# Kernel optimization log

Measured on AMD Instinct MI355X. Metric: run time of the kernel, lower is better.

Reference implementation:

```python
import jax, jax.numpy as jnp
import numpy as np

N = 100000      # nodes
E = 1600000     # edges
D_IN, D_H, D_OUT = 256, 64, 47


def setup_inputs() -> dict:
    key = jax.random.key(0)
    k0, k1, k2, k3 = jax.random.split(key, 4)
    x = jax.random.normal(k0, (N, D_IN), dtype=jnp.float32)
    edge_index = jax.random.randint(k1, (2, E), 0, N, dtype=jnp.int64)
    W1 = jax.random.normal(k2, (D_IN, D_H), dtype=jnp.float32) / np.sqrt(D_IN)
    b1 = jnp.zeros((D_H,), dtype=jnp.float32)
    W2 = jax.random.normal(k3, (D_H, D_OUT), dtype=jnp.float32) / np.sqrt(D_H)
    b2 = jnp.zeros((D_OUT,), dtype=jnp.float32)
    return {"x": x, "edge_index": edge_index, "W1": W1, "b1": b1, "W2": W2, "b2": b2}


def _gcn_conv(x, W, b, src, dst, norm):
    # PyG GCNConv: h = x @ W, then scatter_add(norm * h[src] -> dst), + bias
    h = x @ W                                     # [N, out]
    msg = norm[:, None] * h[src]                  # [E+N, out] gather
    out = jax.ops.segment_sum(msg, dst, num_segments=N)  # scatter-add
    return out + b


def reference(x, edge_index, W1, b1, W2, b2):
    # add self-loops with weight 1 (PyG default, edge_weight=None -> ones)
    loop = jnp.arange(N, dtype=edge_index.dtype)
    src = jnp.concatenate([edge_index[0], loop])
    dst = jnp.concatenate([edge_index[1], loop])
    w = jnp.ones((E + N,), dtype=x.dtype)
    # symmetric normalization: deg^-1/2[src] * w * deg^-1/2[dst]
    deg = jax.ops.segment_sum(w, dst, num_segments=N)
    dinv = jnp.where(deg > 0, jax.lax.rsqrt(deg), 0.0)
    norm = dinv[src] * w * dinv[dst]              # [E+N]

    h = _gcn_conv(x, W1, b1, src, dst, norm)
    h = jax.nn.relu(h)
    # F.dropout(training=self.training): eval mode -> identity
    xo = _gcn_conv(h, W2, b2, src, dst, norm)     # [N, D_OUT]
    logits = jax.nn.softmax(xo, axis=1)           # nn.Softmax() -> dim=1 for 2D
    preds = jnp.argmax(logits, axis=1)
    return (logits, preds, xo)
```

## Files before the change

kernel.cpp:

```cpp
#include <hip/hip_runtime.h>
#include <math.h>

#define NN 100000
#define NE 1600000
#define DI 256
#define DH 64
#define DO 47
#define DH3 48
#define PAD 48
#define RSZ8 ((NN + 7) / 8)
#define EPB 2048
#define CPB ((NE + EPB - 1) / EPB)

__global__ __launch_bounds__(256) void k_fill1(const int* __restrict__ src,
                                               const int* __restrict__ dst,
                                               int* __restrict__ deg,
                                               int* __restrict__ csr_pad) {
    int r = blockIdx.x & 7;
    int chunk = blockIdx.x >> 3;
    int lo = r * RSZ8, hi = min(lo + RSZ8, NN);
    int base = chunk * EPB + threadIdx.x;
    #pragma unroll
    for (int i = 0; i < EPB / 256; ++i) {
        int e = base + i * 256;
        if (e < NE) {
            int d = dst[e];
            if (d >= lo && d < hi) {
                int p = atomicAdd(&deg[d], 1);
                if (p < PAD) csr_pad[d * PAD + p] = src[e];
            }
        }
    }
}

__global__ __launch_bounds__(512) void k_gemm1(const float* __restrict__ x,
                                               const float* __restrict__ W1,
                                               const int* __restrict__ deg,
                                               float* __restrict__ h1s) {
    __shared__ float xs[2][128 * 33];
    __shared__ float wl[2][32 * 64];
    const int t = threadIdx.x;
    const int lane = t & 63;
    const int wvu = __builtin_amdgcn_readfirstlane(t >> 6);
    const int r0 = blockIdx.x * 128;
    const int sr = t >> 2;
    const int sk = (t & 3) * 8;
    const int wk = t >> 4;
    const int wc = (t & 15) * 4;
    const long xrow = (long)min(r0 + sr, NN - 1) * DI;
    const int rowA = r0 + lane;
    const int rowB = r0 + 64 + lane;

    float accA[8] = {0.f, 0.f, 0.f, 0.f, 0.f, 0.f, 0.f, 0.f};
    float accB[8] = {0.f, 0.f, 0.f, 0.f, 0.f, 0.f, 0.f, 0.f};

    {
        float4 v0 = *(const float4*)(x + xrow + sk);
        float4 v1 = *(const float4*)(x + xrow + sk + 4);
        float* p = &xs[0][sr * 33 + sk];
        p[0] = v0.x; p[1] = v0.y; p[2] = v0.z; p[3] = v0.w;
        p[4] = v1.x; p[5] = v1.y; p[6] = v1.z; p[7] = v1.w;
        float4 w = *(const float4*)(W1 + (size_t)wk * DH + wc);
        float* q = &wl[0][wk * 64 + wc];
        q[0] = w.x; q[1] = w.y; q[2] = w.z; q[3] = w.w;
    }
    __syncthreads();
    for (int c = 0; c < 8; ++c) {
        const int buf = c & 1;
        if (c + 1 < 8) {
            float4 v0 = *(const float4*)(x + xrow + (c + 1) * 32 + sk);
            float4 v1 = *(const float4*)(x + xrow + (c + 1) * 32 + sk + 4);
            float* p = &xs[buf ^ 1][sr * 33 + sk];
            p[0] = v0.x; p[1] = v0.y; p[2] = v0.z; p[3] = v0.w;
            p[4] = v1.x; p[5] = v1.y; p[6] = v1.z; p[7] = v1.w;
            float4 w = *(const float4*)(W1 + (size_t)((c + 1) * 32 + wk) * DH + wc);
            float* q = &wl[buf ^ 1][wk * 64 + wc];
            q[0] = w.x; q[1] = w.y; q[2] = w.z; q[3] = w.w;
        }
        #pragma unroll 4
        for (int kk = 0; kk < 32; ++kk) {
            float xa = xs[buf][lane * 33 + kk];
            float xb = xs[buf][(lane + 64) * 33 + kk];
            const float4* wp = (const float4*)&wl[buf][kk * 64 + wvu * 8];
            float4 wa = wp[0], wb = wp[1];
            accA[0] += wa.x * xa; accA[1] += wa.y * xa;
            accA[2] += wa.z * xa; accA[3] += wa.w * xa;
            accA[4] += wb.x * xa; accA[5] += wb.y * xa;
            accA[6] += wb.z * xa; accA[7] += wb.w * xa;
            accB[0] += wa.x * xb; accB[1] += wa.y * xb;
            accB[2] += wa.z * xb; accB[3] += wa.w * xb;
            accB[4] += wb.x * xb; accB[5] += wb.y * xb;
            accB[6] += wb.z * xb; accB[7] += wb.w * xb;
        }
        __syncthreads();
    }
    if (rowA < NN) {
        float di = rsqrtf((float)(deg[rowA] + 1));
        float4 o0 = {di * accA[0], di * accA[1], di * accA[2], di * accA[3]};
        float4 o1 = {di * accA[4], di * accA[5], di * accA[6], di * accA[7]};
        float4* hp = (float4*)(h1s + (long)rowA * DH + wvu * 8);
        hp[0] = o0;
        hp[1] = o1;
    }
    if (rowB < NN) {
        float di = rsqrtf((float)(deg[rowB] + 1));
        float4 o0 = {di * accB[0], di * accB[1], di * accB[2], di * accB[3]};
        float4 o1 = {di * accB[4], di * accB[5], di * accB[6], di * accB[7]};
        float4* hp = (float4*)(h1s + (long)rowB * DH + wvu * 8);
        hp[0] = o0;
        hp[1] = o1;
    }
}

__global__ __launch_bounds__(256) void k_agg1(const int* __restrict__ deg,
                                              const int* __restrict__ csr_pad,
                                              const float* __restrict__ h1s,
                                              const float* __restrict__ b1,
                                              const float* __restrict__ W2,
                                              float* __restrict__ h3s) {
    __shared__ float w2[DH * DO];
    __shared__ float sh[8][DH];
    for (int i = threadIdx.x; i < DH * DO; i += 256) w2[i] = W2[i];
    __syncthreads();
    const int wv = threadIdx.x >> 6, lane = threadIdx.x & 63;
    const int c = lane & 15, e = lane >> 4;
    const unsigned c4 = (unsigned)(c * 4);
    const int rA = blockIdx.x * 8 + wv * 2, rB = rA + 1;
    const int degA = deg[rA], degB = deg[rB];
    const int cntA = min(degA, PAD), cntB = min(degB, PAD);
    const unsigned baseA = (unsigned)rA * PAD, baseB = (unsigned)rB * PAD;
    float aAx = 0.f, aAy = 0.f, aAz = 0.f, aAw = 0.f;
    float aBx = 0.f, aBy = 0.f, aBz = 0.f, aBw = 0.f;
    const int cmin = min(cntA, cntB), tmax = max(cntA, cntB);
    int j = 0;
    for (; j + 7 < cmin; j += 8) {
        unsigned sa0 = (unsigned)csr_pad[baseA + j + e];
        unsigned sb0 = (unsigned)csr_pad[baseB + j + e];
        unsigned sa1 = (unsigned)csr_pad[baseA + j + 4 + e];
        unsigned sb1 = (unsigned)csr_pad[baseB + j + 4 + e];
        float4 va0 = *(const float4*)(h1s + sa0 * 64u + c4);
        float4 vb0 = *(const float4*)(h1s + sb0 * 64u + c4);
        float4 va1 = *(const float4*)(h1s + sa1 * 64u + c4);
        float4 vb1 = *(const float4*)(h1s + sb1 * 64u + c4);
        aAx += va0.x + va1.x; aAy += va0.y + va1.y;
        aAz += va0.z + va1.z; aAw += va0.w + va1.w;
        aBx += vb0.x + vb1.x; aBy += vb0.y + vb1.y;
        aBz += vb0.z + vb1.z; aBw += vb0.w + vb1.w;
    }
    for (; j < tmax; j += 4) {
        int slot = min(j + e, PAD - 1);
        unsigned sa = min((unsigned)csr_pad[baseA + slot], (unsigned)(NN - 1));
        unsigned sb = min((unsigned)csr_pad[baseB + slot], (unsigned)(NN - 1));
        float4 va = *(const float4*)(h1s + sa * 64u + c4);
        float4 vb = *(const float4*)(h1s + sb * 64u + c4);
        float mA = (j + e < cntA) ? 1.f : 0.f;
        float mB = (j + e < cntB) ? 1.f : 0.f;
        aAx = fmaf(mA, va.x, aAx); aAy = fmaf(mA, va.y, aAy);
        aAz = fmaf(mA, va.z, aAz); aAw = fmaf(mA, va.w, aAw);
        aBx = fmaf(mB, vb.x, aBx); aBy = fmaf(mB, vb.y, aBy);
        aBz = fmaf(mB, vb.z, aBz); aBw = fmaf(mB, vb.w, aBw);
    }
    aAx += __shfl_xor(aAx, 16); aAx += __shfl_xor(aAx, 32);
    aAy += __shfl_xor(aAy, 16); aAy += __shfl_xor(aAy, 32);
    aAz += __shfl_xor(aAz, 16); aAz += __shfl_xor(aAz, 32);
    aAw += __shfl_xor(aAw, 16); aAw += __shfl_xor(aAw, 32);
    aBx += __shfl_xor(aBx, 16); aBx += __shfl_xor(aBx, 32);
    aBy += __shfl_xor(aBy, 16); aBy += __shfl_xor(aBy, 32);
    aBz += __shfl_xor(aBz, 16); aBz += __shfl_xor(aBz, 32);
    aBw += __shfl_xor(aBw, 16); aBw += __shfl_xor(aBw, 32);
    const float diA = rsqrtf((float)(degA + 1));
    const float diB = rsqrtf((float)(degB + 1));
    if (lane < 16) {
        float4 sA = *(const float4*)(h1s + (unsigned)rA * 64u + c4);
        float4 sB = *(const float4*)(h1s + (unsigned)rB * 64u + c4);
        float4 bb = *(const float4*)(b1 + c4);
        float4 oA, oB;
        oA.x = fmaxf(diA * (aAx + sA.x) + bb.x, 0.f);
        oA.y = fmaxf(diA * (aAy + sA.y) + bb.y, 0.f);
        oA.z = fmaxf(diA * (aAz + sA.z) + bb.z, 0.f);
        oA.w = fmaxf(diA * (aAw + sA.w) + bb.w, 0.f);
        oB.x = fmaxf(diB * (aBx + sB.x) + bb.x, 0.f);
        oB.y = fmaxf(diB * (aBy + sB.y) + bb.y, 0.f);
        oB.z = fmaxf(diB * (aBz + sB.z) + bb.z, 0.f);
        oB.w = fmaxf(diB * (aBw + sB.w) + bb.w, 0.f);
        *(float4*)&sh[wv * 2 + 0][c4] = oA;
        *(float4*)&sh[wv * 2 + 1][c4] = oB;
    }
    __syncthreads();
    if (lane < DO) {
        float oA = 0.f, oB = 0.f;
        #pragma unroll 8
        for (int k = 0; k < DH; ++k) {
            float w = w2[k * DO + lane];
            oA += sh[wv * 2 + 0][k] * w;
            oB += sh[wv * 2 + 1][k] * w;
        }
        h3s[(unsigned)rA * DH3 + lane] = diA * oA;
        h3s[(unsigned)rB * DH3 + lane] = diB * oB;
    }
}

__global__ __launch_bounds__(256) void k_agg2(const int* __restrict__ deg,
                                              const int* __restrict__ csr_pad,
                                              const float* __restrict__ h3s,
                                              const float* __restrict__ b2,
                                              float* __restrict__ logits,
                                              float* __restrict__ preds,
                                              float* __restrict__ xo) {
    const int wv = threadIdx.x >> 6, lane = threadIdx.x & 63;
    const int c = lane & 15, e = lane >> 4;
    const unsigned cc4 = (unsigned)(((c < 12) ? c : 0) * 4);
    const int rA = blockIdx.x * 8 + wv * 2, rB = rA + 1;
    const int degA = deg[rA], degB = deg[rB];
    const int cntA = min(degA, PAD), cntB = min(degB, PAD);
    const unsigned baseA = (unsigned)rA * PAD, baseB = (unsigned)rB * PAD;
    float aAx = 0.f, aAy = 0.f, aAz = 0.f, aAw = 0.f;
    float aBx = 0.f, aBy = 0.f, aBz = 0.f, aBw = 0.f;
    const int cmin = min(cntA, cntB), tmax = max(cntA, cntB);
    int j = 0;
    for (; j + 7 < cmin; j += 8) {
        unsigned sa0 = (unsigned)csr_pad[baseA + j + e];
        unsigned sb0 = (unsigned)csr_pad[baseB + j + e];
        unsigned sa1 = (unsigned)csr_pad[baseA + j + 4 + e];
        unsigned sb1 = (unsigned)csr_pad[baseB + j + 4 + e];
        float4 va0 = *(const float4*)(h3s + sa0 * 48u + cc4);
        float4 vb0 = *(const float4*)(h3s + sb0 * 48u + cc4);
        float4 va1 = *(const float4*)(h3s + sa1 * 48u + cc4);
        float4 vb1 = *(const float4*)(h3s + sb1 * 48u + cc4);
        aAx += va0.x + va1.x; aAy += va0.y + va1.y;
        aAz += va0.z + va1.z; aAw += va0.w + va1.w;
        aBx += vb0.x + vb1.x; aBy += vb0.y + vb1.y;
        aBz += vb0.z + vb1.z; aBw += vb0.w + vb1.w;
    }
    for (; j < tmax; j += 4) {
        int slot = min(j + e, PAD - 1);
        unsigned sa = min((unsigned)csr_pad[baseA + slot], (unsigned)(NN - 1));
        unsigned sb = min((unsigned)csr_pad[baseB + slot], (unsigned)(NN - 1));
        float4 va = *(const float4*)(h3s + sa * 48u + cc4);
        float4 vb = *(const float4*)(h3s + sb * 48u + cc4);
        float mA = (j + e < cntA) ? 1.f : 0.f;
        float mB = (j + e < cntB) ? 1.f : 0.f;
        aAx = fmaf(mA, va.x, aAx); aAy = fmaf(mA, va.y, aAy);
        aAz = fmaf(mA, va.z, aAz); aAw = fmaf(mA, va.w, aAw);
        aBx = fmaf(mB, vb.x, aBx); aBy = fmaf(mB, vb.y, aBy);
        aBz = fmaf(mB, vb.z, aBz); aBw = fmaf(mB, vb.w, aBw);
    }
    aAx += __shfl_xor(aAx, 16); aAx += __shfl_xor(aAx, 32);
    aAy += __shfl_xor(aAy, 16); aAy += __shfl_xor(aAy, 32);
    aAz += __shfl_xor(aAz, 16); aAz += __shfl_xor(aAz, 32);
    aAw += __shfl_xor(aAw, 16); aAw += __shfl_xor(aAw, 32);
    aBx += __shfl_xor(aBx, 16); aBx += __shfl_xor(aBx, 32);
    aBy += __shfl_xor(aBy, 16); aBy += __shfl_xor(aBy, 32);
    aBz += __shfl_xor(aBz, 16); aBz += __shfl_xor(aBz, 32);
    aBw += __shfl_xor(aBw, 16); aBw += __shfl_xor(aBw, 32);
    const float diA = rsqrtf((float)(degA + 1));
    const float diB = rsqrtf((float)(degB + 1));
    const bool lv = (lane < 16) && (c < 12);
    float b0 = 0.f, bq1 = 0.f, bq2 = 0.f, bq3 = 0.f;
    if (lv) {
        b0 = b2[c * 4 + 0]; bq1 = b2[c * 4 + 1]; bq2 = b2[c * 4 + 2];
        bq3 = (c < 11) ? b2[c * 4 + 3] : 0.f;
    }
    #pragma unroll
    for (int rr = 0; rr < 2; ++rr) {
        const int row = rr ? rB : rA;
        const float di = rr ? diB : diA;
        float ax = rr ? aBx : aAx, ay = rr ? aBy : aAy;
        float az = rr ? aBz : aAz, aw = rr ? aBw : aAw;
        float vx = -INFINITY, vy = -INFINITY, vz = -INFINITY, vw = -INFINITY;
        if (lv) {
            float4 sf = *(const float4*)(h3s + (unsigned)row * 48u + cc4);
            vx = di * (ax + sf.x) + b0;
            vy = di * (ay + sf.y) + bq1;
            vz = di * (az + sf.z) + bq2;
            vw = (c < 11) ? (di * (aw + sf.w) + bq3) : -INFINITY;
            float* xp = xo + (size_t)row * DO + c * 4;
            xp[0] = vx; xp[1] = vy; xp[2] = vz;
            if (c < 11) xp[3] = vw;
        }
        float lm = fmaxf(fmaxf(vx, vy), fmaxf(vz, vw));
        float gm = lm;
        for (int off = 32; off; off >>= 1) gm = fmaxf(gm, __shfl_xor(gm, off));
        int cand = 1 << 30;
        if (lv) {
            if (vx == gm) cand = c * 4 + 0;
            else if (vy == gm) cand = c * 4 + 1;
            else if (vz == gm) cand = c * 4 + 2;
            else if (c < 11 && vw == gm) cand = c * 4 + 3;
        }
        for (int off = 32; off; off >>= 1) cand = min(cand, __shfl_xor(cand, off));
        float e0 = 0.f, e1 = 0.f, e2 = 0.f, e3 = 0.f;
        if (lv) {
            e0 = expf(vx - gm); e1 = expf(vy - gm); e2 = expf(vz - gm);
            e3 = (c < 11) ? expf(vw - gm) : 0.f;
        }
        float gs = e0 + e1 + e2 + e3;
        for (int off = 32; off; off >>= 1) gs += __shfl_xor(gs, off);
        if (lv) {
            float* lp = logits + (size_t)row * DO + c * 4;
            lp[0] = e0 / gs; lp[1] = e1 / gs; lp[2] = e2 / gs;
            if (c < 11) lp[3] = e3 / gs;
        }
        if (lane == 0) preds[row] = (float)cand;
    }
}

extern "C" void kernel_launch(void* const* d_in, const int* in_sizes, int n_in,
                              void* d_out, int out_size, void* d_ws, size_t ws_size,
                              hipStream_t stream) {
    const float* x  = (const float*)d_in[0];
    const int*   ei = (const int*)d_in[1];
    const float* W1 = (const float*)d_in[2];
    const float* b1 = (const float*)d_in[3];
    const float* W2 = (const float*)d_in[4];
    const float* b2 = (const float*)d_in[5];
    const int* src = ei;
    const int* dst = ei + NE;

    float* out    = (float*)d_out;
    float* logits = out;
    float* preds  = out + (size_t)NN * DO;
    float* xo     = preds + NN;

    char* wsb = (char*)d_ws;
    int*   deg     = (int*)wsb;                         wsb += (size_t)NN * 4;
    int*   csr_pad = (int*)wsb;                         wsb += (size_t)NN * PAD * 4;
    float* h1s     = (float*)wsb;                       wsb += (size_t)NN * DH * 4;
    float* h3s     = (float*)wsb;                       wsb += (size_t)NN * DH3 * 4;

    hipMemsetAsync(deg, 0, NN * sizeof(int), stream);

    k_fill1<<<8 * CPB, 256, 0, stream>>>(src, dst, deg, csr_pad);
    k_gemm1<<<(NN + 127) / 128, 512, 0, stream>>>(x, W1, deg, h1s);
    k_agg1<<<NN / 8, 256, 0, stream>>>(deg, csr_pad, h1s, b1, W2, h3s);
    k_agg2<<<NN / 8, 256, 0, stream>>>(deg, csr_pad, h3s, b2, logits, preds, xo);
}
```

Before: 291.7 us.

## Sort nodes by degree and aggregate four same-degree rows per wave

Adds a degree histogram, prefix scan and counting sort that builds a node order grouped by in-degree. Both aggregation kernels now have each wave handle four rows taken from that order instead of two consecutive rows. Rows in a wave then have similar neighbour counts, which cuts the masked tail iterations and raises the number of independent gathers in flight. The cost is three extra small kernel launches and scattered, non-coalesced output writes, since rows are processed in permuted order.

Measured after the change: 577.9 us. 98.1% more time.

```diff
diff --git a/kernel.cpp b/kernel.cpp
--- a/kernel.cpp
+++ b/kernel.cpp
@@ -8,6 +8,8 @@
 #define DO 47
 #define DH3 48
 #define PAD 48
+#define BINS 64
+#define NB ((NN + 255) / 256)
 #define RSZ8 ((NN + 7) / 8)
 #define EPB 2048
 #define CPB ((NE + EPB - 1) / EPB)
@@ -30,6 +32,39 @@
                 if (p < PAD) csr_pad[d * PAD + p] = src[e];
             }
         }
+    }
+}
+
+__global__ __launch_bounds__(256) void k_hist(const int* __restrict__ deg,
+                                              int* __restrict__ bins) {
+    __shared__ int lb[BINS];
+    if (threadIdx.x < BINS) lb[threadIdx.x] = 0;
+    __syncthreads();
+    int i = blockIdx.x * 256 + threadIdx.x;
+    if (i < NN) atomicAdd(&lb[min(deg[i], BINS - 1)], 1);
+    __syncthreads();
+    if (threadIdx.x < BINS && lb[threadIdx.x])
+        atomicAdd(&bins[threadIdx.x], lb[threadIdx.x]);
+}
+
+__global__ __launch_bounds__(64) void k_prefix(int* __restrict__ bins) {
+    int t = threadIdx.x;
+    int v0 = bins[t];
+    int v = v0;
+    for (int off = 1; off < 64; off <<= 1) {
+        int u = __shfl_up(v, off);
+        if (t >= off) v += u;
+    }
+    bins[t] = v - v0;
+}
+
+__global__ __launch_bounds__(256) void k_order(const int* __restrict__ deg,
+                                               int* __restrict__ bins,
+                                               int* __restrict__ order) {
+    int i = blockIdx.x * 256 + threadIdx.x;
+    if (i < NN) {
+        int p = atomicAdd(&bins[min(deg[i], BINS - 1)], 1);
+        order[p] = i;
     }
 }
 
@@ -113,94 +148,96 @@
 }
 
 __global__ __launch_bounds__(256) void k_agg1(const int* __restrict__ deg,
+                                              const int* __restrict__ order,
                                               const int* __restrict__ csr_pad,
                                               const float* __restrict__ h1s,
                                               const float* __restrict__ b1,
                                               const float* __restrict__ W2,
                                               float* __restrict__ h3s) {
     __shared__ float w2[DH * DO];
-    __shared__ float sh[8][DH];
+    __shared__ float sh[16][DH];
     for (int i = threadIdx.x; i < DH * DO; i += 256) w2[i] = W2[i];
     __syncthreads();
     const int wv = threadIdx.x >> 6, lane = threadIdx.x & 63;
     const int c = lane & 15, e = lane >> 4;
     const unsigned c4 = (unsigned)(c * 4);
-    const int rA = blockIdx.x * 8 + wv * 2, rB = rA + 1;
-    const int degA = deg[rA], degB = deg[rB];
-    const int cntA = min(degA, PAD), cntB = min(degB, PAD);
-    const unsigned baseA = (unsigned)rA * PAD, baseB = (unsigned)rB * PAD;
-    float aAx = 0.f, aAy = 0.f, aAz = 0.f, aAw = 0.f;
-    float aBx = 0.f, aBy = 0.f, aBz = 0.f, aBw = 0.f;
-    const int cmin = min(cntA, cntB), tmax = max(cntA, cntB);
+    const int qbase = blockIdx.x * 16 + wv * 4;
+    int row[4], dg[4], cnt[4];
+    unsigned base[4];
+    #pragma unroll
+    for (int r = 0; r < 4; ++r) {
+        row[r] = order[qbase + r];
+        dg[r] = deg[row[r]];
+        cnt[r] = min(dg[r], PAD);
+        base[r] = (unsigned)row[r] * PAD;
+    }
+    float ax[4] = {0.f, 0.f, 0.f, 0.f}, ay[4] = {0.f, 0.f, 0.f, 0.f};
+    float az[4] = {0.f, 0.f, 0.f, 0.f}, aw[4] = {0.f, 0.f, 0.f, 0.f};
+    const int cmin = min(min(cnt[0], cnt[1]), min(cnt[2], cnt[3]));
+    const int tmax = max(max(cnt[0], cnt[1]), max(cnt[2], cnt[3]));
     int j = 0;
     for (; j + 7 < cmin; j += 8) {
-        unsigned sa0 = (unsigned)csr_pad[baseA + j + e];
-        unsigned sb0 = (unsigned)csr_pad[baseB + j + e];
-        unsigned sa1 = (unsigned)csr_pad[baseA + j + 4 + e];
-        unsigned sb1 = (unsigned)csr_pad[baseB + j + 4 + e];
-        float4 va0 = *(const float4*)(h1s + sa0 * 64u + c4);
-        float4 vb0 = *(const float4*)(h1s + sb0 * 64u + c4);
-        float4 va1 = *(const float4*)(h1s + sa1 * 64u + c4);
-        float4 vb1 = *(const float4*)(h1s + sb1 * 64u + c4);
-        aAx += va0.x + va1.x; aAy += va0.y + va1.y;
-        aAz += va0.z + va1.z; aAw += va0.w + va1.w;
-        aBx += vb0.x + vb1.x; aBy += vb0.y + vb1.y;
-        aBz += vb0.z + vb1.z; aBw += vb0.w + vb1.w;
+        #pragma unroll
+        for (int g = 0; g < 2; ++g) {
+            #pragma unroll
+            for (int r = 0; r < 4; ++r) {
+                unsigned s = (unsigned)csr_pad[base[r] + j + g * 4 + e];
+                float4 v = *(const float4*)(h1s + s * 64u + c4);
+                ax[r] += v.x; ay[r] += v.y; az[r] += v.z; aw[r] += v.w;
+            }
+        }
     }
     for (; j < tmax; j += 4) {
         int slot = min(j + e, PAD - 1);
-        unsigned sa = min((unsigned)csr_pad[baseA + slot], (unsigned)(NN - 1));
-        unsigned sb = min((unsigned)csr_pad[baseB + slot], (unsigned)(NN - 1));
-        float4 va = *(const float4*)(h1s + sa * 64u + c4);
-        float4 vb = *(const float4*)(h1s + sb * 64u + c4);
-        float mA = (j + e < cntA) ? 1.f : 0.f;
-        float mB = (j + e < cntB) ? 1.f : 0.f;
-        aAx = fmaf(mA, va.x, aAx); aAy = fmaf(mA, va.y, aAy);
-        aAz = fmaf(mA, va.z, aAz); aAw = fmaf(mA, va.w, aAw);
-        aBx = fmaf(mB, vb.x, aBx); aBy = fmaf(mB, vb.y, aBy);
-        aBz = fmaf(mB, vb.z, aBz); aBw = fmaf(mB, vb.w, aBw);
-    }
-    aAx += __shfl_xor(aAx, 16); aAx += __shfl_xor(aAx, 32);
-    aAy += __shfl_xor(aAy, 16); aAy += __shfl_xor(aAy, 32);
-    aAz += __shfl_xor(aAz, 16); aAz += __shfl_xor(aAz, 32);
-    aAw += __shfl_xor(aAw, 16); aAw += __shfl_xor(aAw, 32);
-    aBx += __shfl_xor(aBx, 16); aBx += __shfl_xor(aBx, 32);
-    aBy += __shfl_xor(aBy, 16); aBy += __shfl_xor(aBy, 32);
-    aBz += __shfl_xor(aBz, 16); aBz += __shfl_xor(aBz, 32);
-    aBw += __shfl_xor(aBw, 16); aBw += __shfl_xor(aBw, 32);
-    const float diA = rsqrtf((float)(degA + 1));
-    const float diB = rsqrtf((float)(degB + 1));
+        #pragma unroll
+        for (int r = 0; r < 4; ++r) {
+            unsigned s = min((unsigned)csr_pad[base[r] + slot], (unsigned)(NN - 1));
+            float4 v = *(const float4*)(h1s + s * 64u + c4);
+            float m = (j + e < cnt[r]) ? 1.f : 0.f;
+            ax[r] = fmaf(m, v.x, ax[r]); ay[r] = fmaf(m, v.y, ay[r]);
+            az[r] = fmaf(m, v.z, az[r]); aw[r] = fmaf(m, v.w, aw[r]);
+        }
+    }
+    #pragma unroll
+    for (int r = 0; r < 4; ++r) {
+        ax[r] += __shfl_xor(ax[r], 16); ax[r] += __shfl_xor(ax[r], 32);
+        ay[r] += __shfl_xor(ay[r], 16); ay[r] += __shfl_xor(ay[r], 32);
+        az[r] += __shfl_xor(az[r], 16); az[r] += __shfl_xor(az[r], 32);
+        aw[r] += __shfl_xor(aw[r], 16); aw[r] += __shfl_xor(aw[r], 32);
+    }
     if (lane < 16) {
-        float4 sA = *(const float4*)(h1s + (unsigned)rA * 64u + c4);
-        float4 sB = *(const float4*)(h1s + (unsigned)rB * 64u + c4);
         float4 bb = *(const float4*)(b1 + c4);
-        float4 oA, oB;
-        oA.x = fmaxf(diA * (aAx + sA.x) + bb.x, 0.f);
-        oA.y = fmaxf(diA * (aAy + sA.y) + bb.y, 0.f);
-        oA.z = fmaxf(diA * (aAz + sA.z) + bb.z, 0.f);
-        oA.w = fmaxf(diA * (aAw + sA.w) + bb.w, 0.f);
-        oB.x = fmaxf(diB * (aBx + sB.x) + bb.x, 0.f);
-        oB.y = fmaxf(diB * (aBy + sB.y) + bb.y, 0.f);
-        oB.z = fmaxf(diB * (aBz + sB.z) + bb.z, 0.f);
-        oB.w = fmaxf(diB * (aBw + sB.w) + bb.w, 0.f);
-        *(float4*)&sh[wv * 2 + 0][c4] = oA;
-        *(float4*)&sh[wv * 2 + 1][c4] = oB;
+        #pragma unroll
+        for (int r = 0; r < 4; ++r) {
+            float di = rsqrtf((float)(dg[r] + 1));
+            float4 sf = *(const float4*)(h1s + (unsigned)row[r] * 64u + c4);
+            float4 o;
+            o.x = fmaxf(di * (ax[r] + sf.x) + bb.x, 0.f);
+            o.y = fmaxf(di * (ay[r] + sf.y) + bb.y, 0.f);
+            o.z = fmaxf(di * (az[r] + sf.z) + bb.z, 0.f);
+            o.w = fmaxf(di * (aw[r] + sf.w) + bb.w, 0.f);
+            *(float4*)&sh[wv * 4 + r][c4] = o;
+        }
     }
     __syncthreads();
     if (lane < DO) {
-        float oA = 0.f, oB = 0.f;
+        float o[4] = {0.f, 0.f, 0.f, 0.f};
         #pragma unroll 8
         for (int k = 0; k < DH; ++k) {
             float w = w2[k * DO + lane];
-            oA += sh[wv * 2 + 0][k] * w;
-            oB += sh[wv * 2 + 1][k] * w;
-        }
-        h3s[(unsigned)rA * DH3 + lane] = diA * oA;
-        h3s[(unsigned)rB * DH3 + lane] = diB * oB;
+            #pragma unroll
+            for (int r = 0; r < 4; ++r) o[r] += sh[wv * 4 + r][k] * w;
+        }
+        #pragma unroll
+        for (int r = 0; r < 4; ++r) {
+            float di = rsqrtf((float)(dg[r] + 1));
+            h3s[(unsigned)row[r] * DH3 + lane] = di * o[r];
+        }
     }
 }
 
 __global__ __launch_bounds__(256) void k_agg2(const int* __restrict__ deg,
+                                              const int* __restrict__ order,
                                               const int* __restrict__ csr_pad,
                                               const float* __restrict__ h3s,
                                               const float* __restrict__ b2,
@@ -210,51 +247,50 @@
     const int wv = threadIdx.x >> 6, lane = threadIdx.x & 63;
     const int c = lane & 15, e = lane >> 4;
     const unsigned cc4 = (unsigned)(((c < 12) ? c : 0) * 4);
-    const int rA = blockIdx.x * 8 + wv * 2, rB = rA + 1;
-    const int degA = deg[rA], degB = deg[rB];
-    const int cntA = min(degA, PAD), cntB = min(degB, PAD);
-    const unsigned baseA = (unsigned)rA * PAD, baseB = (unsigned)rB * PAD;
-    float aAx = 0.f, aAy = 0.f, aAz = 0.f, aAw = 0.f;
-    float aBx = 0.f, aBy = 0.f, aBz = 0.f, aBw = 0.f;
-    const int cmin = min(cntA, cntB), tmax = max(cntA, cntB);
+    const int qbase = blockIdx.x * 16 + wv * 4;
+    int row[4], dg[4], cnt[4];
+    unsigned base[4];
+    #pragma unroll
+    for (int r = 0; r < 4; ++r) {
+        row[r] = order[qbase + r];
+        dg[r] = deg[row[r]];
+        cnt[r] = min(dg[r], PAD);
+        base[r] = (unsigned)row[r] * PAD;
+    }
+    float ax[4] = {0.f, 0.f, 0.f, 0.f}, ay[4] = {0.f, 0.f, 0.f, 0.f};
+    float az[4] = {0.f, 0.f, 0.f, 0.f}, aw[4] = {0.f, 0.f, 0.f, 0.f};
+    const int cmin = min(min(cnt[0], cnt[1]), min(cnt[2], cnt[3]));
+    const int tmax = max(max(cnt[0], cnt[1]), max(cnt[2], cnt[3]));
     int j = 0;
     for (; j + 7 < cmin; j += 8) {
-        unsigned sa0 = (unsigned)csr_pad[baseA + j + e];
-        unsigned sb0 = (unsigned)csr_pad[baseB + j + e];
-        unsigned sa1 = (unsigned)csr_pad[baseA + j + 4 + e];
-        unsigned sb1 = (unsigned)csr_pad[baseB + j + 4 + e];
-        float4 va0 = *(const float4*)(h3s + sa0 * 48u + cc4);
-        float4 vb0 = *(const float4*)(h3s + sb0 * 48u + cc4);
-        float4 va1 = *(const float4*)(h3s + sa1 * 48u + cc4);
-        float4 vb1 = *(const float4*)(h3s + sb1 * 48u + cc4);
-        aAx += va0.x + va1.x; aAy += va0.y + va1.y;
-        aAz += va0.z + va1.z; aAw += va0.w + va1.w;
-        aBx += vb0.x + vb1.x; aBy += vb0.y + vb1.y;
-        aBz += vb0.z + vb1.z; aBw += vb0.w + vb1.w;
+        #pragma unroll
+        for (int g = 0; g < 2; ++g) {
+            #pragma unroll
+            for (int r = 0; r < 4; ++r) {
+                unsigned s = (unsigned)csr_pad[base[r] + j + g * 4 + e];
+                float4 v = *(const float4*)(h3s + s * 48u + cc4);
+                ax[r] += v.x; ay[r] += v.y; az[r] += v.z; aw[r] += v.w;
+            }
+        }
     }
     for (; j < tmax; j += 4) {
         int slot = min(j + e, PAD - 1);
-        unsigned sa = min((unsigned)csr_pad[baseA + slot], (unsigned)(NN - 1));
-        unsigned sb = min((unsigned)csr_pad[baseB + slot], (unsigned)(NN - 1));
-        float4 va = *(const float4*)(h3s + sa * 48u + cc4);
-        float4 vb = *(const float4*)(h3s + sb * 48u + cc4);
-        float mA = (j + e < cntA) ? 1.f : 0.f;
-        float mB = (j + e < cntB) ? 1.f : 0.f;
-        aAx = fmaf(mA, va.x, aAx); aAy = fmaf(mA, va.y, aAy);
-        aAz = fmaf(mA, va.z, aAz); aAw = fmaf(mA, va.w, aAw);
-        aBx = fmaf(mB, vb.x, aBx); aBy = fmaf(mB, vb.y, aBy);
-        aBz = fmaf(mB, vb.z, aBz); aBw = fmaf(mB, vb.w, aBw);
-    }
-    aAx += __shfl_xor(aAx, 16); aAx += __shfl_xor(aAx, 32);
-    aAy += __shfl_xor(aAy, 16); aAy += __shfl_xor(aAy, 32);
-    aAz += __shfl_xor(aAz, 16); aAz += __shfl_xor(aAz, 32);
-    aAw += __shfl_xor(aAw, 16); aAw += __shfl_xor(aAw, 32);
-    aBx += __shfl_xor(aBx, 16); aBx += __shfl_xor(aBx, 32);
-    aBy += __shfl_xor(aBy, 16); aBy += __shfl_xor(aBy, 32);
-    aBz += __shfl_xor(aBz, 16); aBz += __shfl_xor(aBz, 32);
-    aBw += __shfl_xor(aBw, 16); aBw += __shfl_xor(aBw, 32);
-    const float diA = rsqrtf((float)(degA + 1));
-    const float diB = rsqrtf((float)(degB + 1));
+        #pragma unroll
+        for (int r = 0; r < 4; ++r) {
+            unsigned s = min((unsigned)csr_pad[base[r] + slot], (unsigned)(NN - 1));
+            float4 v = *(const float4*)(h3s + s * 48u + cc4);
+            float m = (j + e < cnt[r]) ? 1.f : 0.f;
+            ax[r] = fmaf(m, v.x, ax[r]); ay[r] = fmaf(m, v.y, ay[r]);
+            az[r] = fmaf(m, v.z, az[r]); aw[r] = fmaf(m, v.w, aw[r]);
+        }
+    }
+    #pragma unroll
+    for (int r = 0; r < 4; ++r) {
+        ax[r] += __shfl_xor(ax[r], 16); ax[r] += __shfl_xor(ax[r], 32);
+        ay[r] += __shfl_xor(ay[r], 16); ay[r] += __shfl_xor(ay[r], 32);
+        az[r] += __shfl_xor(az[r], 16); az[r] += __shfl_xor(az[r], 32);
+        aw[r] += __shfl_xor(aw[r], 16); aw[r] += __shfl_xor(aw[r], 32);
+    }
     const bool lv = (lane < 16) && (c < 12);
     float b0 = 0.f, bq1 = 0.f, bq2 = 0.f, bq3 = 0.f;
     if (lv) {
@@ -262,24 +298,21 @@
         bq3 = (c < 11) ? b2[c * 4 + 3] : 0.f;
     }
     #pragma unroll
-    for (int rr = 0; rr < 2; ++rr) {
-        const int row = rr ? rB : rA;
-        const float di = rr ? diB : diA;
-        float ax = rr ? aBx : aAx, ay = rr ? aBy : aAy;
-        float az = rr ? aBz : aAz, aw = rr ? aBw : aAw;
+    for (int r = 0; r < 4; ++r) {
+        const int rw = row[r];
+        const float di = rsqrtf((float)(dg[r] + 1));
         float vx = -INFINITY, vy = -INFINITY, vz = -INFINITY, vw = -INFINITY;
         if (lv) {
-            float4 sf = *(const float4*)(h3s + (unsigned)row * 48u + cc4);
-            vx = di * (ax + sf.x) + b0;
-            vy = di * (ay + sf.y) + bq1;
-            vz = di * (az + sf.z) + bq2;
-            vw = (c < 11) ? (di * (aw + sf.w) + bq3) : -INFINITY;
-            float* xp = xo + (size_t)row * DO + c * 4;
+            float4 sf = *(const float4*)(h3s + (unsigned)rw * 48u + cc4);
+            vx = di * (ax[r] + sf.x) + b0;
+            vy = di * (ay[r] + sf.y) + bq1;
+            vz = di * (az[r] + sf.z) + bq2;
+            vw = (c < 11) ? (di * (aw[r] + sf.w) + bq3) : -INFINITY;
+            float* xp = xo + (size_t)rw * DO + c * 4;
             xp[0] = vx; xp[1] = vy; xp[2] = vz;
             if (c < 11) xp[3] = vw;
         }
-        float lm = fmaxf(fmaxf(vx, vy), fmaxf(vz, vw));
-        float gm = lm;
+        float gm = fmaxf(fmaxf(vx, vy), fmaxf(vz, vw));
         for (int off = 32; off; off >>= 1) gm = fmaxf(gm, __shfl_xor(gm, off));
         int cand = 1 << 30;
         if (lv) {
@@ -297,11 +330,11 @@
         float gs = e0 + e1 + e2 + e3;
         for (int off = 32; off; off >>= 1) gs += __shfl_xor(gs, off);
         if (lv) {
-            float* lp = logits + (size_t)row * DO + c * 4;
+            float* lp = logits + (size_t)rw * DO + c * 4;
             lp[0] = e0 / gs; lp[1] = e1 / gs; lp[2] = e2 / gs;
             if (c < 11) lp[3] = e3 / gs;
         }
-        if (lane == 0) preds[row] = (float)cand;
+        if (lane == 0) preds[rw] = (float)cand;
     }
 }
 
@@ -324,14 +357,19 @@
 
     char* wsb = (char*)d_ws;
     int*   deg     = (int*)wsb;                         wsb += (size_t)NN * 4;
+    int*   bins    = (int*)wsb;                         wsb += (size_t)BINS * 4;
+    int*   order   = (int*)wsb;                         wsb += (size_t)NN * 4;
     int*   csr_pad = (int*)wsb;                         wsb += (size_t)NN * PAD * 4;
     float* h1s     = (float*)wsb;                       wsb += (size_t)NN * DH * 4;
     float* h3s     = (float*)wsb;                       wsb += (size_t)NN * DH3 * 4;
 
-    hipMemsetAsync(deg, 0, NN * sizeof(int), stream);
+    hipMemsetAsync(deg, 0, ((size_t)NN + BINS) * sizeof(int), stream);
 
     k_fill1<<<8 * CPB, 256, 0, stream>>>(src, dst, deg, csr_pad);
+    k_hist<<<NB, 256, 0, stream>>>(deg, bins);
+    k_prefix<<<1, 64, 0, stream>>>(bins);
+    k_order<<<NB, 256, 0, stream>>>(deg, bins, order);
     k_gemm1<<<(NN + 127) / 128, 512, 0, stream>>>(x, W1, deg, h1s);
-    k_agg1<<<NN / 8, 256, 0, stream>>>(deg, csr_pad, h1s, b1, W2, h3s);
-    k_agg2<<<NN / 8, 256, 0, stream>>>(deg, csr_pad, h3s, b2, logits, preds, xo);
-}
+    k_agg1<<<NN / 16, 256, 0, stream>>>(deg, order, csr_pad, h1s, b1, W2, h3s);
+    k_agg2<<<NN / 16, 256, 0, stream>>>(deg, order, csr_pad, h3s, b2, logits, preds, xo);
+}
```
